# Kernel optimization log

Measured on AMD Instinct MI355X. Metric: run time of the kernel, lower is better.

## Reference

```python
import jax, jax.numpy as jnp
import numpy as np

CHNN = 1024
K = 2048


def _conv1x1(W, b, x):
    # x: (B, C_in, L), W: (C_out, C_in), b: (C_out,)
    return jnp.einsum('oc,bcl->bol', W, x) + b[None, :, None]


def setup_inputs() -> dict:
    key = jax.random.key(0)
    ks = jax.random.split(key, 10)
    s = 0.02
    return {
        'vc': jax.random.normal(ks[0], (1, CHNN, K), dtype=jnp.float32),
        'vm': jax.random.normal(ks[1], (1, CHNN, K), dtype=jnp.float32),
        'W_ak': jax.random.normal(ks[2], (K, CHNN), dtype=jnp.float32) * s,
        'b_ak': jax.random.normal(ks[3], (K,), dtype=jnp.float32) * s,
        'W_c': jax.random.normal(ks[4], (CHNN, CHNN), dtype=jnp.float32) * s,
        'b_c': jax.random.normal(ks[5], (CHNN,), dtype=jnp.float32) * s,
        'W_mad': jax.random.normal(ks[6], (CHNN, CHNN), dtype=jnp.float32) * s,
        'b_mad': jax.random.normal(ks[7], (CHNN,), dtype=jnp.float32) * s,
        'W_gcn': jax.random.normal(ks[8], (CHNN, CHNN), dtype=jnp.float32) * s,
        'b_gcn': jax.random.normal(ks[9], (CHNN,), dtype=jnp.float32) * s,
    }


def reference(vc, vm, W_ak, b_ak, W_c, b_c, W_mad, b_mad, W_gcn, b_gcn):
    # vcw: (1, K, L) assignment logits; softmax over the K (channel) dim
    vcw = _conv1x1(W_ak, b_ak, vc)
    vcw = jax.nn.softmax(vcw, axis=1)
    w = vcw[0].T                      # (L, K)  (batch forced to 1 by squeeze(0))
    # vm features: (1, CHNN, K)
    vmr = jax.nn.relu(_conv1x1(W_c, b_c, vm))
    # F.linear(vm, w): contract last dim (K) with w's second dim -> (1, CHNN, L)
    vma = jnp.einsum('bck,lk->bcl', vmr, w)
    vma = _conv1x1(W_mad, b_mad, vma)  # (1, CHNN, L)
    # dense adjacency over positions: (1, L, L)
    A = jnp.einsum('bck,bcl->bkl', vma, vma)
    # GCN: x (1, K, CHNN) @ W + b, then softmax(A) @ x  (requires L == K)
    x = jnp.swapaxes(vmr, 1, 2) @ W_gcn + b_gcn
    A = jax.nn.softmax(A, axis=-1)
    out = A @ x                        # (1, L, CHNN)
    return jnp.swapaxes(out, 1, 2)     # (1, CHNN, L)
```

## Files before the change

### kernel.cpp

```cpp
#include <hip/hip_runtime.h>
#include <hip/hip_bf16.h>


typedef __bf16 bf16x4 __attribute__((ext_vector_type(4)));
typedef __bf16 bf16x8 __attribute__((ext_vector_type(8)));
typedef float  f32x4  __attribute__((ext_vector_type(4)));

typedef const void __attribute__((address_space(1)))* gptr_t;
typedef void       __attribute__((address_space(3)))* lptr_t;

__device__ __forceinline__ void load16_lds(const __bf16* g, __bf16* l)
{
    __builtin_amdgcn_global_load_lds((gptr_t)g, (lptr_t)l, 16, 0, 0);
}

#define WAITCNT_VM8 0x0F78
#define WAITCNT_VM0 0x0F70

template<typename OT, int BIAS_, bool RELU_, int STORE_>
struct GC {
    using OUT_T = OT;
    static constexpr int BIAS = BIAS_, STORE = STORE_;
    static constexpr bool RELU = RELU_;
};

template<class CF>
__device__ __forceinline__ void gemm_body(
    int bid, __bf16* sA, __bf16* sB,
    const __bf16* __restrict__ A, const __bf16* __restrict__ B,
    const float* __restrict__ bias,
    typename CF::OUT_T* __restrict__ C, typename CF::OUT_T* __restrict__ CT,
    int M, int N, int K, int ntx)
{
    const int lane = threadIdx.x & 63;
    const int m0 = (bid / ntx) * 64, n0 = (bid % ntx) * 64;
    const __bf16* gA = A + (size_t)m0 * K;
    const __bf16* gB = B + (size_t)n0 * K;

    f32x4 acc[4][4];
    #pragma unroll
    for (int i = 0; i < 4; ++i)
        #pragma unroll
        for (int j = 0; j < 4; ++j)
            acc[i][j] = (f32x4){0.f, 0.f, 0.f, 0.f};

    auto stage = [&](int k0, int buf) {
        #pragma unroll
        for (int i = 0; i < 4; ++i) {
            const int c = i * 64 + lane;
            load16_lds(gA + (size_t)(c >> 2) * K + k0 + (c & 3) * 8,
                       &sA[buf * 2048 + i * 512]);
        }
        #pragma unroll
        for (int i = 0; i < 4; ++i) {
            const int c = i * 64 + lane;
            load16_lds(gB + (size_t)(c >> 2) * K + k0 + (c & 3) * 8,
                       &sB[buf * 2048 + i * 512]);
        }
    };

    stage(0, 0);
    stage(32, 1);
    int cur = 0;
    for (int k0 = 0; k0 < K - 32; k0 += 32) {
        __builtin_amdgcn_s_waitcnt(WAITCNT_VM8);
        bf16x8 af[4], bfr[4];
        #pragma unroll
        for (int i = 0; i < 4; ++i) {
            af[i]  = *(const bf16x8*)&sA[cur * 2048 + (i * 16 + (lane & 15)) * 32 + (lane >> 4) * 8];
            bfr[i] = *(const bf16x8*)&sB[cur * 2048 + (i * 16 + (lane & 15)) * 32 + (lane >> 4) * 8];
        }
        #pragma unroll
        for (int i = 0; i < 4; ++i)
            #pragma unroll
            for (int j = 0; j < 4; ++j)
                acc[i][j] = __builtin_amdgcn_mfma_f32_16x16x32_bf16(af[i], bfr[j], acc[i][j], 0, 0, 0);
        if (k0 + 64 < K) stage(k0 + 64, cur);
        cur ^= 1;
    }
    __builtin_amdgcn_s_waitcnt(WAITCNT_VM0);
    {
        bf16x8 af[4], bfr[4];
        #pragma unroll
        for (int i = 0; i < 4; ++i) {
            af[i]  = *(const bf16x8*)&sA[cur * 2048 + (i * 16 + (lane & 15)) * 32 + (lane >> 4) * 8];
            bfr[i] = *(const bf16x8*)&sB[cur * 2048 + (i * 16 + (lane & 15)) * 32 + (lane >> 4) * 8];
        }
        #pragma unroll
        for (int i = 0; i < 4; ++i)
            #pragma unroll
            for (int j = 0; j < 4; ++j)
                acc[i][j] = __builtin_amdgcn_mfma_f32_16x16x32_bf16(af[i], bfr[j], acc[i][j], 0, 0, 0);
    }

    #pragma unroll
    for (int i = 0; i < 4; ++i) {
        const int rowb = m0 + i * 16 + (lane >> 4) * 4;
        #pragma unroll
        for (int j = 0; j < 4; ++j) {
            const int col = n0 + j * 16 + (lane & 15);
            f32x4 v = acc[i][j];
            #pragma unroll
            for (int r = 0; r < 4; ++r) {
                float f = v[r];
                if (CF::BIAS == 1) f += bias[rowb + r];
                if (CF::BIAS == 2) f += bias[col];
                if (CF::RELU) f = fmaxf(f, 0.f);
                v[r] = f;
            }
            if (CF::STORE == 0) {
                #pragma unroll
                for (int r = 0; r < 4; ++r)
                    C[(size_t)(rowb + r) * N + col] = (typename CF::OUT_T)v[r];
            } else {
                if constexpr (sizeof(typename CF::OUT_T) == 4) {
                    *(f32x4*)&CT[(size_t)col * M + rowb] = v;
                } else {
                    bf16x4 w = { (__bf16)v[0], (__bf16)v[1], (__bf16)v[2], (__bf16)v[3] };
                    *(bf16x4*)&CT[(size_t)col * M + rowb] = w;
                }
            }
        }
    }
}

__device__ __forceinline__ void softmax_row_w(__bf16* __restrict__ p)
{
    const int lane = threadIdx.x & 63;
    bf16x8 v[4];
    float f[32];
    #pragma unroll
    for (int r = 0; r < 4; ++r)
        v[r] = *(const bf16x8*)&p[(r * 64 + lane) * 8];
    float m = -1e30f;
    #pragma unroll
    for (int r = 0; r < 4; ++r)
        #pragma unroll
        for (int j = 0; j < 8; ++j) {
            f[r * 8 + j] = (float)v[r][j];
            m = fmaxf(m, f[r * 8 + j]);
        }
    #pragma unroll
    for (int s = 1; s < 64; s <<= 1) m = fmaxf(m, __shfl_xor(m, s, 64));
    float sum = 0.f;
    #pragma unroll
    for (int i = 0; i < 32; ++i) { f[i] = expf(f[i] - m); sum += f[i]; }
    #pragma unroll
    for (int s = 1; s < 64; s <<= 1) sum += __shfl_xor(sum, s, 64);
    const float inv = 1.f / sum;
    #pragma unroll
    for (int r = 0; r < 4; ++r) {
        bf16x8 w;
        #pragma unroll
        for (int j = 0; j < 8; ++j) w[j] = (__bf16)(f[r * 8 + j] * inv);
        *(bf16x8*)&p[(r * 64 + lane) * 8] = w;
    }
}

template<class CF>
__global__ __launch_bounds__(64, 2)
void gemm1w(const __bf16* __restrict__ A, const __bf16* __restrict__ B,
            const float* __restrict__ bias,
            typename CF::OUT_T* __restrict__ C, typename CF::OUT_T* __restrict__ CT,
            int M, int N, int K, int ntx)
{
    __shared__ __bf16 sAB[8192];
    gemm_body<CF>(blockIdx.x, sAB, sAB + 4096, A, B, bias, C, CT, M, N, K, ntx);
}

template<class C1, class C2>
__global__ __launch_bounds__(64, 2)
void gemm2w(int nblk1,
            const __bf16* __restrict__ A1, const __bf16* __restrict__ B1,
            const float* __restrict__ b1,
            typename C1::OUT_T* __restrict__ C1p, typename C1::OUT_T* __restrict__ CT1,
            int M1, int N1, int K1, int ntx1,
            const __bf16* __restrict__ A2, const __bf16* __restrict__ B2,
            const float* __restrict__ b2,
            typename C2::OUT_T* __restrict__ C2p, typename C2::OUT_T* __restrict__ CT2,
            int M2, int N2, int K2, int ntx2)
{
    __shared__ __bf16 sAB[8192];
    const int b = blockIdx.x;
    if (b < nblk1)
        gemm_body<C1>(b, sAB, sAB + 4096, A1, B1, b1, C1p, CT1, M1, N1, K1, ntx1);
    else
        gemm_body<C2>(b - nblk1, sAB, sAB + 4096, A2, B2, b2, C2p, CT2, M2, N2, K2, ntx2);
}

template<class C1, class C2>
__global__ __launch_bounds__(64, 2)
void gemm2smw(int nblk1, int nblk2,
              const __bf16* __restrict__ A1, const __bf16* __restrict__ B1,
              const float* __restrict__ b1, typename C1::OUT_T* __restrict__ C1p,
              int M1, int N1, int K1, int ntx1,
              const __bf16* __restrict__ A2, const __bf16* __restrict__ B2,
              const float* __restrict__ b2, typename C2::OUT_T* __restrict__ C2p,
              int M2, int N2, int K2, int ntx2,
              __bf16* __restrict__ SM)
{
    __shared__ __bf16 sAB[8192];
    const int b = blockIdx.x;
    if (b < nblk1)
        gemm_body<C1>(b, sAB, sAB + 4096, A1, B1, b1, C1p,
                      (typename C1::OUT_T*)nullptr, M1, N1, K1, ntx1);
    else if (b < nblk1 + nblk2)
        gemm_body<C2>(b - nblk1, sAB, sAB + 4096, A2, B2, b2, C2p,
                      (typename C2::OUT_T*)nullptr, M2, N2, K2, ntx2);
    else
        softmax_row_w(SM + (size_t)(b - nblk1 - nblk2) * 2048);
}

__global__ __launch_bounds__(64)
void row_softmax_w(__bf16* __restrict__ A)
{
    softmax_row_w(A + (size_t)blockIdx.x * 2048);
}

__device__ __forceinline__ void tp_tile(const float* __restrict__ in,
                                        __bf16* __restrict__ outp,
                                        int R, int C, int bx, int by)
{
    __shared__ float t[32][33];
    const int tx = threadIdx.x & 31, ty = threadIdx.x >> 5;
    #pragma unroll
    for (int i = ty; i < 32; i += 8)
        t[i][tx] = in[(size_t)(by + i) * C + (bx + tx)];
    __syncthreads();
    #pragma unroll
    for (int i = ty; i < 32; i += 8)
        outp[(size_t)(bx + i) * R + (by + tx)] = (__bf16)t[tx][i];
}

__device__ __forceinline__ void cast_blk(const float* __restrict__ s,
                                         __bf16* __restrict__ d, int blk)
{
    const int i = blk * 1024 + threadIdx.x * 4;
    float4 v = *(const float4*)&s[i];
    bf16x4 w = { (__bf16)v.x, (__bf16)v.y, (__bf16)v.z, (__bf16)v.w };
    *(bf16x4*)&d[i] = w;
}

__global__ __launch_bounds__(256)
void prep(const float* __restrict__ vc, __bf16* __restrict__ vcT,
          const float* __restrict__ vm, __bf16* __restrict__ vmT,
          const float* __restrict__ W_ak, __bf16* __restrict__ W_akb,
          const float* __restrict__ W_c, __bf16* __restrict__ W_cb,
          const float* __restrict__ W_mad, __bf16* __restrict__ W_madb,
          const float* __restrict__ W_gcn, __bf16* __restrict__ W_gcnT)
{
    const int x = blockIdx.x;
    if (blockIdx.z == 0) {
        const float* in = (x < 2048) ? vc : vm;
        __bf16* o       = (x < 2048) ? vcT : vmT;
        const int e = x & 2047;
        tp_tile(in, o, 1024, 2048, (e & 63) * 32, (e >> 6) * 32);
    } else if (blockIdx.z == 1) {
        if (x < 2048)      cast_blk(W_ak, W_akb, x);
        else if (x < 3072) cast_blk(W_c, W_cb, x - 2048);
        else               cast_blk(W_mad, W_madb, x - 3072);
    } else {
        if (x >= 1024) return;
        tp_tile(W_gcn, W_gcnT, 1024, 1024, (x & 31) * 32, (x >> 5) * 32);
    }
}

extern "C" void kernel_launch(void* const* d_in, const int* in_sizes, int n_in,
                              void* d_out, int out_size, void* d_ws, size_t ws_size,
                              hipStream_t stream)
{
    const float* vc    = (const float*)d_in[0];
    const float* vm    = (const float*)d_in[1];
    const float* W_ak  = (const float*)d_in[2];
    const float* b_ak  = (const float*)d_in[3];
    const float* W_c   = (const float*)d_in[4];
    const float* b_c   = (const float*)d_in[5];
    const float* W_mad = (const float*)d_in[6];
    const float* b_mad = (const float*)d_in[7];
    const float* W_gcn = (const float*)d_in[8];
    const float* b_gcn = (const float*)d_in[9];
    float* out = (float*)d_out;

    char* ws = (char*)d_ws;
    const size_t MB = 1u << 20;
    __bf16* ST     = (__bf16*)(ws);
    __bf16* P      = (__bf16*)(ws);
    __bf16* vcT    = (__bf16*)(ws + 8 * MB);
    __bf16* vmaT   = (__bf16*)(ws + 8 * MB);
    __bf16* W_akb  = (__bf16*)(ws + 12 * MB);
    __bf16* vmm    = (__bf16*)(ws + 12 * MB);
    __bf16* vmT    = (__bf16*)(ws + 16 * MB);
    __bf16* xT     = (__bf16*)(ws + 16 * MB);
    __bf16* W_cb   = (__bf16*)(ws + 20 * MB);
    __bf16* W_madb = (__bf16*)(ws + 22 * MB);
    __bf16* vmrT   = (__bf16*)(ws + 24 * MB);
    __bf16* W_gcnT = (__bf16*)(ws + 28 * MB);

    using G3  = GC<__bf16, 2, false, 0>;
    using G5  = GC<__bf16, 1, true,  1>;
    using G6  = GC<__bf16, 0, false, 0>;
    using G11 = GC<__bf16, 1, false, 0>;
    using G7  = GC<__bf16, 2, false, 0>;
    using G9  = GC<__bf16, 0, false, 0>;
    using G12 = GC<float,  0, false, 1>;

    prep<<<dim3(4096, 1, 3), 256, 0, stream>>>(vc, vcT, vm, vmT, W_ak, W_akb,
                                               W_c, W_cb, W_mad, W_madb,
                                               W_gcn, W_gcnT);
    gemm2w<G3, G5><<<1536, 64, 0, stream>>>(1024,
        vcT, W_akb, b_ak, ST, (__bf16*)nullptr, 2048, 2048, 1024, 32,
        W_cb, vmT, b_c, (__bf16*)nullptr, vmrT, 1024, 2048, 1024, 32);
    gemm2smw<G6, G11><<<3072, 64, 0, stream>>>(512, 512,
        W_madb, vmrT, nullptr, vmm, 1024, 2048, 1024, 32,
        W_gcnT, vmrT, b_gcn, xT, 1024, 2048, 1024, 32,
        ST);
    gemm1w<G7><<<512, 64, 0, stream>>>(ST, vmm, b_mad, vmaT, (__bf16*)nullptr,
                                       2048, 1024, 2048, 16);
    gemm1w<G9><<<1024, 64, 0, stream>>>(vmaT, vmaT, nullptr, P, (__bf16*)nullptr,
                                        2048, 2048, 1024, 32);
    row_softmax_w<<<2048, 64, 0, stream>>>(P);
    gemm1w<G12><<<512, 64, 0, stream>>>(P, xT, nullptr, (float*)nullptr, out,
                                        2048, 1024, 2048, 16);
}
```

Measured before the change: 208.2 us.

## Load GEMM operands straight to registers and remap tiles per XCD for L2 locality

Drops the LDS staging path, where global_load_lds double-buffered A/B tiles. Each lane now loads its MFMA fragments directly from global memory into registers, double-buffered two k-steps of 32 ahead. Block-to-tile mapping becomes XCD-aware: blockIdx low bits pick the XCD, and each XCD gets a contiguous PMxPN patch of tiles so the chiplet's L2 sees more reuse. This also removes the shared-memory footprint and the occupancy hint. The cost is uncoalesced 16-byte strided global loads with no cross-wave sharing inside a CU, which relies on cache hits.

```diff
diff --git a/kernel.cpp b/kernel.cpp
--- a/kernel.cpp
+++ b/kernel.cpp
@@ -6,100 +6,88 @@
 typedef __bf16 bf16x8 __attribute__((ext_vector_type(8)));
 typedef float  f32x4  __attribute__((ext_vector_type(4)));
 
-typedef const void __attribute__((address_space(1)))* gptr_t;
-typedef void       __attribute__((address_space(3)))* lptr_t;
-
-__device__ __forceinline__ void load16_lds(const __bf16* g, __bf16* l)
-{
-    __builtin_amdgcn_global_load_lds((gptr_t)g, (lptr_t)l, 16, 0, 0);
-}
-
-#define WAITCNT_VM8 0x0F78
-#define WAITCNT_VM0 0x0F70
-
-template<typename OT, int BIAS_, bool RELU_, int STORE_>
+template<typename OT, int BIAS_, bool RELU_, int STORE_, int PM_, int PN_, int NPC_>
 struct GC {
     using OUT_T = OT;
     static constexpr int BIAS = BIAS_, STORE = STORE_;
     static constexpr bool RELU = RELU_;
+    static constexpr int PM = PM_, PN = PN_, NPC = NPC_;
 };
 
 template<class CF>
 __device__ __forceinline__ void gemm_body(
-    int bid, __bf16* sA, __bf16* sB,
+    int bid,
     const __bf16* __restrict__ A, const __bf16* __restrict__ B,
     const float* __restrict__ bias,
     typename CF::OUT_T* __restrict__ C, typename CF::OUT_T* __restrict__ CT,
-    int M, int N, int K, int ntx)
+    int M, int N, int K)
 {
     const int lane = threadIdx.x & 63;
-    const int m0 = (bid / ntx) * 64, n0 = (bid % ntx) * 64;
-    const __bf16* gA = A + (size_t)m0 * K;
-    const __bf16* gB = B + (size_t)n0 * K;
+    const int xcd = bid & 7, j = bid >> 3;
+    const int pr = xcd / CF::NPC, pc = xcd % CF::NPC;
+    const int jm = j / CF::PN, jn = j % CF::PN;
+    const int m0 = (pr * CF::PM + jm) * 64;
+    const int n0 = (pc * CF::PN + jn) * 64;
+
+    const __bf16* pA = A + (size_t)(m0 + (lane & 15)) * K + (lane >> 4) * 8;
+    const __bf16* pB = B + (size_t)(n0 + (lane & 15)) * K + (lane >> 4) * 8;
 
     f32x4 acc[4][4];
     #pragma unroll
     for (int i = 0; i < 4; ++i)
         #pragma unroll
-        for (int j = 0; j < 4; ++j)
-            acc[i][j] = (f32x4){0.f, 0.f, 0.f, 0.f};
-
-    auto stage = [&](int k0, int buf) {
-        #pragma unroll
-        for (int i = 0; i < 4; ++i) {
-            const int c = i * 64 + lane;
-            load16_lds(gA + (size_t)(c >> 2) * K + k0 + (c & 3) * 8,
-                       &sA[buf * 2048 + i * 512]);
-        }
-        #pragma unroll
-        for (int i = 0; i < 4; ++i) {
-            const int c = i * 64 + lane;
-            load16_lds(gB + (size_t)(c >> 2) * K + k0 + (c & 3) * 8,
-                       &sB[buf * 2048 + i * 512]);
-        }
-    };
-
-    stage(0, 0);
-    stage(32, 1);
-    int cur = 0;
-    for (int k0 = 0; k0 < K - 32; k0 += 32) {
-        __builtin_amdgcn_s_waitcnt(WAITCNT_VM8);
-        bf16x8 af[4], bfr[4];
-        #pragma unroll
-        for (int i = 0; i < 4; ++i) {
-            af[i]  = *(const bf16x8*)&sA[cur * 2048 + (i * 16 + (lane & 15)) * 32 + (lane >> 4) * 8];
-            bfr[i] = *(const bf16x8*)&sB[cur * 2048 + (i * 16 + (lane & 15)) * 32 + (lane >> 4) * 8];
-        }
+        for (int jj = 0; jj < 4; ++jj)
+            acc[i][jj] = (f32x4){0.f, 0.f, 0.f, 0.f};
+
+    bf16x8 a0[4], b0[4], a1[4], b1[4];
+    #pragma unroll
+    for (int i = 0; i < 4; ++i) {
+        a0[i] = *(const bf16x8*)(pA + (size_t)(i * 16) * K);
+        b0[i] = *(const bf16x8*)(pB + (size_t)(i * 16) * K);
+        a1[i] = *(const bf16x8*)(pA + (size_t)(i * 16) * K + 32);
+        b1[i] = *(const bf16x8*)(pB + (size_t)(i * 16) * K + 32);
+    }
+
+    for (int k0 = 0; k0 < K - 64; k0 += 64) {
         #pragma unroll
         for (int i = 0; i < 4; ++i)
             #pragma unroll
-            for (int j = 0; j < 4; ++j)
-                acc[i][j] = __builtin_amdgcn_mfma_f32_16x16x32_bf16(af[i], bfr[j], acc[i][j], 0, 0, 0);
-        if (k0 + 64 < K) stage(k0 + 64, cur);
-        cur ^= 1;
-    }
-    __builtin_amdgcn_s_waitcnt(WAITCNT_VM0);
-    {
-        bf16x8 af[4], bfr[4];
+            for (int jj = 0; jj < 4; ++jj)
+                acc[i][jj] = __builtin_amdgcn_mfma_f32_16x16x32_bf16(a0[i], b0[jj], acc[i][jj], 0, 0, 0);
         #pragma unroll
         for (int i = 0; i < 4; ++i) {
-            af[i]  = *(const bf16x8*)&sA[cur * 2048 + (i * 16 + (lane & 15)) * 32 + (lane >> 4) * 8];
-            bfr[i] = *(const bf16x8*)&sB[cur * 2048 + (i * 16 + (lane & 15)) * 32 + (lane >> 4) * 8];
+            a0[i] = *(const bf16x8*)(pA + (size_t)(i * 16) * K + k0 + 64);
+            b0[i] = *(const bf16x8*)(pB + (size_t)(i * 16) * K + k0 + 64);
         }
         #pragma unroll
         for (int i = 0; i < 4; ++i)
             #pragma unroll
-            for (int j = 0; j < 4; ++j)
-                acc[i][j] = __builtin_amdgcn_mfma_f32_16x16x32_bf16(af[i], bfr[j], acc[i][j], 0, 0, 0);
-    }
+            for (int jj = 0; jj < 4; ++jj)
+                acc[i][jj] = __builtin_amdgcn_mfma_f32_16x16x32_bf16(a1[i], b1[jj], acc[i][jj], 0, 0, 0);
+        #pragma unroll
+        for (int i = 0; i < 4; ++i) {
+            a1[i] = *(const bf16x8*)(pA + (size_t)(i * 16) * K + k0 + 96);
+            b1[i] = *(const bf16x8*)(pB + (size_t)(i * 16) * K + k0 + 96);
+        }
+    }
+    #pragma unroll
+    for (int i = 0; i < 4; ++i)
+        #pragma unroll
+        for (int jj = 0; jj < 4; ++jj)
+            acc[i][jj] = __builtin_amdgcn_mfma_f32_16x16x32_bf16(a0[i], b0[jj], acc[i][jj], 0, 0, 0);
+    #pragma unroll
+    for (int i = 0; i < 4; ++i)
+        #pragma unroll
+        for (int jj = 0; jj < 4; ++jj)
+            acc[i][jj] = __builtin_amdgcn_mfma_f32_16x16x32_bf16(a1[i], b1[jj], acc[i][jj], 0, 0, 0);
 
     #pragma unroll
     for (int i = 0; i < 4; ++i) {
         const int rowb = m0 + i * 16 + (lane >> 4) * 4;
         #pragma unroll
-        for (int j = 0; j < 4; ++j) {
-            const int col = n0 + j * 16 + (lane & 15);
-            f32x4 v = acc[i][j];
+        for (int jj = 0; jj < 4; ++jj) {
+            const int col = n0 + jj * 16 + (lane & 15);
+            f32x4 v = acc[i][jj];
             #pragma unroll
             for (int r = 0; r < 4; ++r) {
                 float f = v[r];
@@ -158,55 +146,50 @@
 }
 
 template<class CF>
-__global__ __launch_bounds__(64, 2)
+__global__ __launch_bounds__(64)
 void gemm1w(const __bf16* __restrict__ A, const __bf16* __restrict__ B,
             const float* __restrict__ bias,
             typename CF::OUT_T* __restrict__ C, typename CF::OUT_T* __restrict__ CT,
-            int M, int N, int K, int ntx)
-{
-    __shared__ __bf16 sAB[8192];
-    gemm_body<CF>(blockIdx.x, sAB, sAB + 4096, A, B, bias, C, CT, M, N, K, ntx);
+            int M, int N, int K)
+{
+    gemm_body<CF>(blockIdx.x, A, B, bias, C, CT, M, N, K);
 }
 
 template<class C1, class C2>
-__global__ __launch_bounds__(64, 2)
+__global__ __launch_bounds__(64)
 void gemm2w(int nblk1,
             const __bf16* __restrict__ A1, const __bf16* __restrict__ B1,
             const float* __restrict__ b1,
             typename C1::OUT_T* __restrict__ C1p, typename C1::OUT_T* __restrict__ CT1,
-            int M1, int N1, int K1, int ntx1,
+            int M1, int N1, int K1,
             const __bf16* __restrict__ A2, const __bf16* __restrict__ B2,
             const float* __restrict__ b2,
             typename C2::OUT_T* __restrict__ C2p, typename C2::OUT_T* __restrict__ CT2,
-            int M2, int N2, int K2, int ntx2)
-{
-    __shared__ __bf16 sAB[8192];
+            int M2, int N2, int K2)
+{
     const int b = blockIdx.x;
     if (b < nblk1)
-        gemm_body<C1>(b, sAB, sAB + 4096, A1, B1, b1, C1p, CT1, M1, N1, K1, ntx1);
+        gemm_body<C1>(b, A1, B1, b1, C1p, CT1, M1, N1, K1);
     else
-        gemm_body<C2>(b - nblk1, sAB, sAB + 4096, A2, B2, b2, C2p, CT2, M2, N2, K2, ntx2);
+        gemm_body<C2>(b - nblk1, A2, B2, b2, C2p, CT2, M2, N2, K2);
 }
 
 template<class C1, class C2>
-__global__ __launch_bounds__(64, 2)
+__global__ __launch_bounds__(64)
 void gemm2smw(int nblk1, int nblk2,
               const __bf16* __restrict__ A1, const __bf16* __restrict__ B1,
               const float* __restrict__ b1, typename C1::OUT_T* __restrict__ C1p,
-              int M1, int N1, int K1, int ntx1,
+              int M1, int N1, int K1,
               const __bf16* __restrict__ A2, const __bf16* __restrict__ B2,
               const float* __restrict__ b2, typename C2::OUT_T* __restrict__ C2p,
-              int M2, int N2, int K2, int ntx2,
+              int M2, int N2, int K2,
               __bf16* __restrict__ SM)
 {
-    __shared__ __bf16 sAB[8192];
     const int b = blockIdx.x;
     if (b < nblk1)
-        gemm_body<C1>(b, sAB, sAB + 4096, A1, B1, b1, C1p,
-                      (typename C1::OUT_T*)nullptr, M1, N1, K1, ntx1);
+        gemm_body<C1>(b, A1, B1, b1, C1p, (typename C1::OUT_T*)nullptr, M1, N1, K1);
     else if (b < nblk1 + nblk2)
-        gemm_body<C2>(b - nblk1, sAB, sAB + 4096, A2, B2, b2, C2p,
-                      (typename C2::OUT_T*)nullptr, M2, N2, K2, ntx2);
+        gemm_body<C2>(b - nblk1, A2, B2, b2, C2p, (typename C2::OUT_T*)nullptr, M2, N2, K2);
     else
         softmax_row_w(SM + (size_t)(b - nblk1 - nblk2) * 2048);
 }
@@ -296,29 +279,29 @@
     __bf16* vmrT   = (__bf16*)(ws + 24 * MB);
     __bf16* W_gcnT = (__bf16*)(ws + 28 * MB);
 
-    using G3  = GC<__bf16, 2, false, 0>;
-    using G5  = GC<__bf16, 1, true,  1>;
-    using G6  = GC<__bf16, 0, false, 0>;
-    using G11 = GC<__bf16, 1, false, 0>;
-    using G7  = GC<__bf16, 2, false, 0>;
-    using G9  = GC<__bf16, 0, false, 0>;
-    using G12 = GC<float,  0, false, 1>;
+    using G3  = GC<__bf16, 2, false, 0,  8, 16, 2>;
+    using G5  = GC<__bf16, 1, true,  1,  8,  8, 4>;
+    using G6  = GC<__bf16, 0, false, 0,  8,  8, 4>;
+    using G11 = GC<__bf16, 1, false, 0,  8,  8, 4>;
+    using G7  = GC<__bf16, 2, false, 0,  8,  8, 2>;
+    using G9  = GC<__bf16, 0, false, 0,  8, 16, 2>;
+    using G12 = GC<float,  0, false, 1,  8,  8, 2>;
 
     prep<<<dim3(4096, 1, 3), 256, 0, stream>>>(vc, vcT, vm, vmT, W_ak, W_akb,
                                                W_c, W_cb, W_mad, W_madb,
                                                W_gcn, W_gcnT);
     gemm2w<G3, G5><<<1536, 64, 0, stream>>>(1024,
-        vcT, W_akb, b_ak, ST, (__bf16*)nullptr, 2048, 2048, 1024, 32,
-        W_cb, vmT, b_c, (__bf16*)nullptr, vmrT, 1024, 2048, 1024, 32);
+        vcT, W_akb, b_ak, ST, (__bf16*)nullptr, 2048, 2048, 1024,
+        W_cb, vmT, b_c, (__bf16*)nullptr, vmrT, 1024, 2048, 1024);
     gemm2smw<G6, G11><<<3072, 64, 0, stream>>>(512, 512,
-        W_madb, vmrT, nullptr, vmm, 1024, 2048, 1024, 32,
-        W_gcnT, vmrT, b_gcn, xT, 1024, 2048, 1024, 32,
+        W_madb, vmrT, nullptr, vmm, 1024, 2048, 1024,
+        W_gcnT, vmrT, b_gcn, xT, 1024, 2048, 1024,
         ST);
     gemm1w<G7><<<512, 64, 0, stream>>>(ST, vmm, b_mad, vmaT, (__bf16*)nullptr,
-                                       2048, 1024, 2048, 16);
+                                       2048, 1024, 2048);
     gemm1w<G9><<<1024, 64, 0, stream>>>(vmaT, vmaT, nullptr, P, (__bf16*)nullptr,
-                                        2048, 2048, 1024, 32);
+                                        2048, 2048, 1024);
     row_softmax_w<<<2048, 64, 0, stream>>>(P);
     gemm1w<G12><<<512, 64, 0, stream>>>(P, xT, nullptr, (float*)nullptr, out,
-                                        2048, 1024, 2048, 16);
-}
+                                        2048, 1024, 2048);
+}
```

Result: slower. 283.0 us (+35.9%).

## Split K of the 2048x2048 GEMMs into two halves and sum them in softmax

Applied to the files above, without the earlier changes.

The two large square GEMMs (the vc assignment logits and the vma self-product adjacency) now each run as two half-K GEMMs writing separate partial outputs. This doubles the block count so more CUs are busy. The partials are summed, with bias added where needed, inside the row softmax that already follows each GEMM. The cost is extra memory traffic, since two bf16 partial matrices are written and read back, plus an extra bf16 rounding of each partial sum. The launch_bounds occupancy hint of 2 is also dropped from the kernels.

```diff
diff --git a/kernel.cpp b/kernel.cpp
--- a/kernel.cpp
+++ b/kernel.cpp
@@ -30,12 +30,12 @@
     const __bf16* __restrict__ A, const __bf16* __restrict__ B,
     const float* __restrict__ bias,
     typename CF::OUT_T* __restrict__ C, typename CF::OUT_T* __restrict__ CT,
-    int M, int N, int K, int ntx)
+    int M, int N, int KLEN, int LDK, int ntx)
 {
     const int lane = threadIdx.x & 63;
     const int m0 = (bid / ntx) * 64, n0 = (bid % ntx) * 64;
-    const __bf16* gA = A + (size_t)m0 * K;
-    const __bf16* gB = B + (size_t)n0 * K;
+    const __bf16* gA = A + (size_t)m0 * LDK;
+    const __bf16* gB = B + (size_t)n0 * LDK;
 
     f32x4 acc[4][4];
     #pragma unroll
@@ -48,13 +48,13 @@
         #pragma unroll
         for (int i = 0; i < 4; ++i) {
             const int c = i * 64 + lane;
-            load16_lds(gA + (size_t)(c >> 2) * K + k0 + (c & 3) * 8,
+            load16_lds(gA + (size_t)(c >> 2) * LDK + k0 + (c & 3) * 8,
                        &sA[buf * 2048 + i * 512]);
         }
         #pragma unroll
         for (int i = 0; i < 4; ++i) {
             const int c = i * 64 + lane;
-            load16_lds(gB + (size_t)(c >> 2) * K + k0 + (c & 3) * 8,
+            load16_lds(gB + (size_t)(c >> 2) * LDK + k0 + (c & 3) * 8,
                        &sB[buf * 2048 + i * 512]);
         }
     };
@@ -62,7 +62,7 @@
     stage(0, 0);
     stage(32, 1);
     int cur = 0;
-    for (int k0 = 0; k0 < K - 32; k0 += 32) {
+    for (int k0 = 0; k0 < KLEN - 32; k0 += 32) {
         __builtin_amdgcn_s_waitcnt(WAITCNT_VM8);
         bf16x8 af[4], bfr[4];
         #pragma unroll
@@ -75,7 +75,7 @@
             #pragma unroll
             for (int j = 0; j < 4; ++j)
                 acc[i][j] = __builtin_amdgcn_mfma_f32_16x16x32_bf16(af[i], bfr[j], acc[i][j], 0, 0, 0);
-        if (k0 + 64 < K) stage(k0 + 64, cur);
+        if (k0 + 64 < KLEN) stage(k0 + 64, cur);
         cur ^= 1;
     }
     __builtin_amdgcn_s_waitcnt(WAITCNT_VM0);
@@ -124,22 +124,26 @@
     }
 }
 
-__device__ __forceinline__ void softmax_row_w(__bf16* __restrict__ p)
+__device__ __forceinline__ void softmax_row2(__bf16* __restrict__ p0,
+                                             const __bf16* __restrict__ p1,
+                                             const float* __restrict__ bias)
 {
     const int lane = threadIdx.x & 63;
-    bf16x8 v[4];
     float f[32];
-    #pragma unroll
-    for (int r = 0; r < 4; ++r)
-        v[r] = *(const bf16x8*)&p[(r * 64 + lane) * 8];
     float m = -1e30f;
     #pragma unroll
-    for (int r = 0; r < 4; ++r)
+    for (int r = 0; r < 4; ++r) {
+        const int base = (r * 64 + lane) * 8;
+        bf16x8 a = *(const bf16x8*)&p0[base];
+        bf16x8 b = *(const bf16x8*)&p1[base];
         #pragma unroll
         for (int j = 0; j < 8; ++j) {
-            f[r * 8 + j] = (float)v[r][j];
-            m = fmaxf(m, f[r * 8 + j]);
-        }
+            float x = (float)a[j] + (float)b[j];
+            if (bias) x += bias[base + j];
+            f[r * 8 + j] = x;
+            m = fmaxf(m, x);
+        }
+    }
     #pragma unroll
     for (int s = 1; s < 64; s <<= 1) m = fmaxf(m, __shfl_xor(m, s, 64));
     float sum = 0.f;
@@ -153,68 +157,94 @@
         bf16x8 w;
         #pragma unroll
         for (int j = 0; j < 8; ++j) w[j] = (__bf16)(f[r * 8 + j] * inv);
-        *(bf16x8*)&p[(r * 64 + lane) * 8] = w;
-    }
-}
-
-template<class CF>
-__global__ __launch_bounds__(64, 2)
-void gemm1w(const __bf16* __restrict__ A, const __bf16* __restrict__ B,
-            const float* __restrict__ bias,
-            typename CF::OUT_T* __restrict__ C, typename CF::OUT_T* __restrict__ CT,
-            int M, int N, int K, int ntx)
-{
-    __shared__ __bf16 sAB[8192];
-    gemm_body<CF>(blockIdx.x, sAB, sAB + 4096, A, B, bias, C, CT, M, N, K, ntx);
-}
-
-template<class C1, class C2>
-__global__ __launch_bounds__(64, 2)
-void gemm2w(int nblk1,
-            const __bf16* __restrict__ A1, const __bf16* __restrict__ B1,
-            const float* __restrict__ b1,
-            typename C1::OUT_T* __restrict__ C1p, typename C1::OUT_T* __restrict__ CT1,
-            int M1, int N1, int K1, int ntx1,
-            const __bf16* __restrict__ A2, const __bf16* __restrict__ B2,
-            const float* __restrict__ b2,
-            typename C2::OUT_T* __restrict__ C2p, typename C2::OUT_T* __restrict__ CT2,
-            int M2, int N2, int K2, int ntx2)
-{
-    __shared__ __bf16 sAB[8192];
+        *(bf16x8*)&p0[(r * 64 + lane) * 8] = w;
+    }
+}
+
+using G3c  = GC<__bf16, 0, false, 0>;
+using G5c  = GC<__bf16, 1, true,  1>;
+using G11c = GC<__bf16, 1, false, 0>;
+using G7c  = GC<__bf16, 2, false, 0>;
+using G12c = GC<float,  0, false, 1>;
+
+__global__ __launch_bounds__(64)
+void k_L2(const __bf16* __restrict__ vcT, const __bf16* __restrict__ W_akb,
+          __bf16* __restrict__ ST0, __bf16* __restrict__ ST1,
+          const __bf16* __restrict__ W_cb, const __bf16* __restrict__ vmT,
+          const float* __restrict__ b_c, __bf16* __restrict__ vmrT)
+{
+    __shared__ __bf16 s[8192];
     const int b = blockIdx.x;
-    if (b < nblk1)
-        gemm_body<C1>(b, sAB, sAB + 4096, A1, B1, b1, C1p, CT1, M1, N1, K1, ntx1);
+    if (b < 1024)
+        gemm_body<G3c>(b, s, s + 4096, vcT, W_akb, nullptr, ST0, (__bf16*)nullptr,
+                       2048, 2048, 512, 1024, 32);
+    else if (b < 2048)
+        gemm_body<G3c>(b - 1024, s, s + 4096, vcT + 512, W_akb + 512, nullptr, ST1,
+                       (__bf16*)nullptr, 2048, 2048, 512, 1024, 32);
     else
-        gemm_body<C2>(b - nblk1, sAB, sAB + 4096, A2, B2, b2, C2p, CT2, M2, N2, K2, ntx2);
-}
-
-template<class C1, class C2>
-__global__ __launch_bounds__(64, 2)
-void gemm2smw(int nblk1, int nblk2,
-              const __bf16* __restrict__ A1, const __bf16* __restrict__ B1,
-              const float* __restrict__ b1, typename C1::OUT_T* __restrict__ C1p,
-              int M1, int N1, int K1, int ntx1,
-              const __bf16* __restrict__ A2, const __bf16* __restrict__ B2,
-              const float* __restrict__ b2, typename C2::OUT_T* __restrict__ C2p,
-              int M2, int N2, int K2, int ntx2,
-              __bf16* __restrict__ SM)
-{
-    __shared__ __bf16 sAB[8192];
+        gemm_body<G5c>(b - 2048, s, s + 4096, W_cb, vmT, b_c, (__bf16*)nullptr,
+                       vmrT, 1024, 2048, 1024, 1024, 32);
+}
+
+__global__ __launch_bounds__(64)
+void k_L3(const __bf16* __restrict__ W_madb, const __bf16* __restrict__ vmrT,
+          __bf16* __restrict__ vmm,
+          const __bf16* __restrict__ W_gcnT, const float* __restrict__ b_gcn,
+          __bf16* __restrict__ xT,
+          __bf16* __restrict__ ST0, const __bf16* __restrict__ ST1,
+          const float* __restrict__ b_ak)
+{
+    __shared__ __bf16 s[8192];
     const int b = blockIdx.x;
-    if (b < nblk1)
-        gemm_body<C1>(b, sAB, sAB + 4096, A1, B1, b1, C1p,
-                      (typename C1::OUT_T*)nullptr, M1, N1, K1, ntx1);
-    else if (b < nblk1 + nblk2)
-        gemm_body<C2>(b - nblk1, sAB, sAB + 4096, A2, B2, b2, C2p,
-                      (typename C2::OUT_T*)nullptr, M2, N2, K2, ntx2);
+    if (b < 512)
+        gemm_body<G3c>(b, s, s + 4096, W_madb, vmrT, nullptr, vmm, (__bf16*)nullptr,
+                       1024, 2048, 1024, 1024, 32);
+    else if (b < 1024)
+        gemm_body<G11c>(b - 512, s, s + 4096, W_gcnT, vmrT, b_gcn, xT,
+                        (__bf16*)nullptr, 1024, 2048, 1024, 1024, 32);
+    else {
+        const size_t row = b - 1024;
+        softmax_row2(ST0 + row * 2048, ST1 + row * 2048, b_ak);
+    }
+}
+
+__global__ __launch_bounds__(64)
+void k_L4(const __bf16* __restrict__ ST, const __bf16* __restrict__ vmm,
+          const float* __restrict__ b_mad, __bf16* __restrict__ vmaT)
+{
+    __shared__ __bf16 s[8192];
+    gemm_body<G7c>(blockIdx.x, s, s + 4096, ST, vmm, b_mad, vmaT,
+                   (__bf16*)nullptr, 2048, 1024, 2048, 2048, 16);
+}
+
+__global__ __launch_bounds__(64)
+void k_L5(const __bf16* __restrict__ vmaT, __bf16* __restrict__ P0,
+          __bf16* __restrict__ P1)
+{
+    __shared__ __bf16 s[8192];
+    const int b = blockIdx.x;
+    if (b < 1024)
+        gemm_body<G3c>(b, s, s + 4096, vmaT, vmaT, nullptr, P0, (__bf16*)nullptr,
+                       2048, 2048, 512, 1024, 32);
     else
-        softmax_row_w(SM + (size_t)(b - nblk1 - nblk2) * 2048);
-}
-
-__global__ __launch_bounds__(64)
-void row_softmax_w(__bf16* __restrict__ A)
-{
-    softmax_row_w(A + (size_t)blockIdx.x * 2048);
+        gemm_body<G3c>(b - 1024, s, s + 4096, vmaT + 512, vmaT + 512, nullptr, P1,
+                       (__bf16*)nullptr, 2048, 2048, 512, 1024, 32);
+}
+
+__global__ __launch_bounds__(64)
+void k_L6(__bf16* __restrict__ P0, const __bf16* __restrict__ P1)
+{
+    const size_t row = blockIdx.x;
+    softmax_row2(P0 + row * 2048, P1 + row * 2048, nullptr);
+}
+
+__global__ __launch_bounds__(64)
+void k_L7(const __bf16* __restrict__ P, const __bf16* __restrict__ xT,
+          float* __restrict__ out)
+{
+    __shared__ __bf16 s[8192];
+    gemm_body<G12c>(blockIdx.x, s, s + 4096, P, xT, nullptr, (float*)nullptr,
+                    out, 2048, 1024, 2048, 2048, 16);
 }
 
 __device__ __forceinline__ void tp_tile(const float* __restrict__ in,
@@ -283,42 +313,29 @@
 
     char* ws = (char*)d_ws;
     const size_t MB = 1u << 20;
-    __bf16* ST     = (__bf16*)(ws);
-    __bf16* P      = (__bf16*)(ws);
-    __bf16* vcT    = (__bf16*)(ws + 8 * MB);
-    __bf16* vmaT   = (__bf16*)(ws + 8 * MB);
-    __bf16* W_akb  = (__bf16*)(ws + 12 * MB);
-    __bf16* vmm    = (__bf16*)(ws + 12 * MB);
-    __bf16* vmT    = (__bf16*)(ws + 16 * MB);
-    __bf16* xT     = (__bf16*)(ws + 16 * MB);
-    __bf16* W_cb   = (__bf16*)(ws + 20 * MB);
-    __bf16* W_madb = (__bf16*)(ws + 22 * MB);
-    __bf16* vmrT   = (__bf16*)(ws + 24 * MB);
-    __bf16* W_gcnT = (__bf16*)(ws + 28 * MB);
-
-    using G3  = GC<__bf16, 2, false, 0>;
-    using G5  = GC<__bf16, 1, true,  1>;
-    using G6  = GC<__bf16, 0, false, 0>;
-    using G11 = GC<__bf16, 1, false, 0>;
-    using G7  = GC<__bf16, 2, false, 0>;
-    using G9  = GC<__bf16, 0, false, 0>;
-    using G12 = GC<float,  0, false, 1>;
+    __bf16* vcT    = (__bf16*)(ws);
+    __bf16* vmT    = (__bf16*)(ws + 4 * MB);
+    __bf16* W_akb  = (__bf16*)(ws + 8 * MB);
+    __bf16* W_cb   = (__bf16*)(ws + 12 * MB);
+    __bf16* W_madb = (__bf16*)(ws + 14 * MB);
+    __bf16* W_gcnT = (__bf16*)(ws + 16 * MB);
+    __bf16* vmrT   = (__bf16*)(ws + 18 * MB);
+    __bf16* ST0    = (__bf16*)(ws + 24 * MB);
+    __bf16* ST1    = (__bf16*)(ws + 32 * MB);
+    __bf16* vmm    = (__bf16*)(ws + 40 * MB);
+    __bf16* xT     = (__bf16*)(ws + 44 * MB);
+    __bf16* vmaT   = (__bf16*)(ws + 48 * MB);
+    __bf16* P0     = (__bf16*)(ws + 56 * MB);
+    __bf16* P1     = (__bf16*)(ws + 64 * MB);
 
     prep<<<dim3(4096, 1, 3), 256, 0, stream>>>(vc, vcT, vm, vmT, W_ak, W_akb,
                                                W_c, W_cb, W_mad, W_madb,
                                                W_gcn, W_gcnT);
-    gemm2w<G3, G5><<<1536, 64, 0, stream>>>(1024,
-        vcT, W_akb, b_ak, ST, (__bf16*)nullptr, 2048, 2048, 1024, 32,
-        W_cb, vmT, b_c, (__bf16*)nullptr, vmrT, 1024, 2048, 1024, 32);
-    gemm2smw<G6, G11><<<3072, 64, 0, stream>>>(512, 512,
-        W_madb, vmrT, nullptr, vmm, 1024, 2048, 1024, 32,
-        W_gcnT, vmrT, b_gcn, xT, 1024, 2048, 1024, 32,
-        ST);
-    gemm1w<G7><<<512, 64, 0, stream>>>(ST, vmm, b_mad, vmaT, (__bf16*)nullptr,
-                                       2048, 1024, 2048, 16);
-    gemm1w<G9><<<1024, 64, 0, stream>>>(vmaT, vmaT, nullptr, P, (__bf16*)nullptr,
-                                        2048, 2048, 1024, 32);
-    row_softmax_w<<<2048, 64, 0, stream>>>(P);
-    gemm1w<G12><<<512, 64, 0, stream>>>(P, xT, nullptr, (float*)nullptr, out,
-                                        2048, 1024, 2048, 16);
-}
+    k_L2<<<2560, 64, 0, stream>>>(vcT, W_akb, ST0, ST1, W_cb, vmT, b_c, vmrT);
+    k_L3<<<3072, 64, 0, stream>>>(W_madb, vmrT, vmm, W_gcnT, b_gcn, xT,
+                                  ST0, ST1, b_ak);
+    k_L4<<<512, 64, 0, stream>>>(ST0, vmm, b_mad, vmaT);
+    k_L5<<<2048, 64, 0, stream>>>(vmaT, P0, P1);
+    k_L6<<<2048, 64, 0, stream>>>(P0, P1);
+    k_L7<<<512, 64, 0, stream>>>(P0, xT, out);
+}
```

Result: slower. 244.5 us (+17.4%).
